# Kernel optimization log

Measured on AMD Instinct MI355X. Metric: run time of the kernel, lower is better.

The kernel has to match this reference:

```python
import jax, jax.numpy as jnp
import numpy as np
from jax import lax

FEAT_STRIDE = 16
RATIOS = np.array([0.5, 1.0, 2.0], np.float32)
SCALES = np.array([8.0, 16.0, 32.0], np.float32)
A = RATIOS.size * SCALES.size            # 9 anchors per location
N_PRE = 3000                             # pre-NMS top-k (TEST-style config)
N_POST = 300                             # post-NMS rois per image
NMS_THRESH = 0.7
MIN_SIZE = 16.0
B, C, HF, WF = 4, 512, 50, 50


def setup_inputs() -> dict:
    key = jax.random.key(0)
    ks = jax.random.split(key, 4)
    mid = 512
    return {
        "inputs": jax.random.normal(ks[0], (B, C, HF, WF), jnp.float32),
        "conv_w": jax.random.normal(ks[1], (mid, C, 3, 3), jnp.float32) * 0.01,
        "conv_b": jnp.zeros((mid,), jnp.float32),
        "bf_w": jax.random.normal(ks[2], (A * 2, mid, 1, 1), jnp.float32) * 0.01,
        "bf_b": jnp.zeros((A * 2,), jnp.float32),
        "loc_w": jax.random.normal(ks[3], (A * 4, mid, 1, 1), jnp.float32) * 0.01,
        "loc_b": jnp.zeros((A * 4,), jnp.float32),
        "img_h": 800,
        "img_w": 800,
    }


def _conv(x, w, b, pad):
    y = lax.conv_general_dilated(x, w, (1, 1), [(pad, pad), (pad, pad)],
                                 dimension_numbers=("NCHW", "OIHW", "NCHW"))
    return y + b[None, :, None, None]


def _anchors(hf, wf):
    ratios = jnp.asarray(RATIOS)
    scales = jnp.asarray(SCALES)
    hs = (FEAT_STRIDE * scales[None, :] * jnp.sqrt(ratios[:, None])).reshape(-1)
    ws = (FEAT_STRIDE * scales[None, :] * jnp.sqrt(1.0 / ratios[:, None])).reshape(-1)
    c = FEAT_STRIDE / 2.0
    base = jnp.stack([c - hs / 2, c - ws / 2, c + hs / 2, c + ws / 2], 1)  # [A,4] yxyx
    sy = jnp.arange(hf, dtype=jnp.float32) * FEAT_STRIDE
    sx = jnp.arange(wf, dtype=jnp.float32) * FEAT_STRIDE
    yy, xx = jnp.meshgrid(sy, sx, indexing="ij")
    shifts = jnp.stack([yy, xx, yy, xx], -1).reshape(-1, 1, 4)
    return (shifts + base[None]).reshape(-1, 4)  # [hf*wf*A, 4]


def _decode(anchors, loc):
    # anchors [N,4] yxyx, loc [B,N,4] (dy,dx,dh,dw)
    ah = anchors[:, 2] - anchors[:, 0]
    aw = anchors[:, 3] - anchors[:, 1]
    acy = anchors[:, 0] + 0.5 * ah
    acx = anchors[:, 1] + 0.5 * aw
    cy = loc[..., 0] * ah + acy
    cx = loc[..., 1] * aw + acx
    h = jnp.exp(loc[..., 2]) * ah
    w = jnp.exp(loc[..., 3]) * aw
    return jnp.stack([cy - 0.5 * h, cx - 0.5 * w, cy + 0.5 * h, cx + 0.5 * w], -1)


def _nms(boxes, scores):
    # boxes [N,4], scores [N] -> fixed-size [N_POST,4] rois (zero-padded)
    hs = boxes[:, 2] - boxes[:, 0]
    ws = boxes[:, 3] - boxes[:, 1]
    valid = (hs >= MIN_SIZE) & (ws >= MIN_SIZE)
    s = jnp.where(valid, scores, -jnp.inf)
    order = jnp.argsort(-s)[:N_PRE]
    b = boxes[order]
    v = valid[order]
    sb = lax.stop_gradient(b)
    area = (sb[:, 2] - sb[:, 0]) * (sb[:, 3] - sb[:, 1])
    tl = jnp.maximum(sb[:, None, :2], sb[None, :, :2])
    br = jnp.minimum(sb[:, None, 2:], sb[None, :, 2:])
    wh = jnp.clip(br - tl, 0.0)
    inter = wh[..., 0] * wh[..., 1]
    iou = inter / (area[:, None] + area[None, :] - inter + 1e-9)

    def body(i, keep):
        sup = jnp.any((iou[i] > NMS_THRESH) & keep)
        return keep.at[i].set(v[i] & ~sup)

    keep = lax.fori_loop(0, N_PRE, body, jnp.zeros((N_PRE,), bool))
    pos = jnp.where(keep, jnp.cumsum(keep) - 1, N_POST)  # invalid -> dropped
    return jnp.zeros((N_POST, 4), boxes.dtype).at[pos].set(b, mode="drop")


def reference(inputs, conv_w, conv_b, bf_w, bf_b, loc_w, loc_b, img_h, img_w):
    b_, _, hf, wf = inputs.shape
    feat = jax.nn.relu(_conv(inputs, conv_w, conv_b, 1))
    loc = _conv(feat, loc_w, loc_b, 0).transpose(0, 2, 3, 1).reshape(b_, -1, 4)
    logits = _conv(feat, bf_w, bf_b, 0).transpose(0, 2, 3, 1).reshape(b_, hf, wf, A, 2)
    probs = jax.nn.softmax(logits, axis=4)
    fg = probs[..., 1].reshape(b_, -1)             # foreground scores [B, hf*wf*A]
    bf_pred = probs.reshape(b_, -1, 2)
    anchors = _anchors(hf, wf)
    boxes = _decode(anchors, loc)
    boxes = jnp.stack([
        jnp.clip(boxes[..., 0], 0.0, img_h), jnp.clip(boxes[..., 1], 0.0, img_w),
        jnp.clip(boxes[..., 2], 0.0, img_h), jnp.clip(boxes[..., 3], 0.0, img_w)], -1)
    rois = jax.vmap(_nms)(boxes, fg).reshape(-1, 4)         # [B*N_POST, 4]
    rois_idx = jnp.repeat(jnp.arange(b_, dtype=jnp.int32), N_POST)
    return rois, rois_idx, anchors, loc, bf_pred
```

## Files before the change

### kernel.cpp

```cpp
#include <hip/hip_runtime.h>
#include <hip/hip_bf16.h>
#include <math.h>

#define BIMG   4
#define CIN    512
#define MID    512
#define HF     50
#define WF     50
#define PIX    2500
#define MTOT   10000
#define ANC    9
#define NLOC   22500
#define NPRE   3000
#define NPOST  300
#define WORDS  47
#define ROWPAD 3008
#define WSTRIDE 48
#define CAP    8192

#define ROIS_OFF 0
#define IDX_OFF  4800
#define ANC_OFF  6000
#define LOC_OFF  96000
#define BF_OFF   456000

#define WS_WT     0UL
#define WS_W1T    9437184UL
#define WS_FEAT   9568256UL
#define WS_SCORE  30048256UL
#define WS_BOXD   30768256UL
#define WS_SBD    33648256UL
#define WS_M      34032256UL
#define WS_CAND   38652544UL
#define WS_CNT    38783616UL
#define WS_PART1  38786048UL
#define WS_PART2  59266048UL
#define WS_PART3  79746048UL
#define WS_NEED2  59266048UL
#define WS_NEED4  100226048UL
#define RAWP_SZ   2560000UL

__global__ __launch_bounds__(256) void prep_kernel(
    const float* __restrict__ conv_w, const float* __restrict__ loc_w,
    const float* __restrict__ bf_w, float* __restrict__ Wt, float* __restrict__ W1t) {
  int o = blockIdx.x * 256 + threadIdx.x;
  if (o < 4608 * 512) {
    int co  = o & 511;
    int k   = o >> 9;
    int c   = k & 511;
    int tap = k >> 9;
    Wt[o] = conv_w[(co * 512 + c) * 9 + tap];
  } else {
    int o2 = o - 4608 * 512;
    if (o2 < 512 * 64) {
      int co = o2 & 63;
      int c  = o2 >> 6;
      float v = 0.0f;
      if (co < 36)      v = loc_w[co * 512 + c];
      else if (co < 54) v = bf_w[(co - 36) * 512 + c];
      W1t[o2] = v;
    }
  }
}

__device__ __forceinline__ void stage_load(
    int kb, int sg, bool in0, bool in1,
    int y0, int x0, int y1, int x1,
    const float* __restrict__ ib0, const float* __restrict__ ib1, float av[8]) {
  int tap = kb >> 5;
  int c0  = (kb & 31) << 4;
  int t3  = tap / 3;
  int dy  = t3 - 1;
  int dx  = tap - t3 * 3 - 1;
  int iy0 = y0 + dy, ix0 = x0 + dx;
  int iy1 = y1 + dy, ix1 = x1 + dx;
  bool ok0 = in0 && ((unsigned)iy0 < (unsigned)HF) && ((unsigned)ix0 < (unsigned)WF);
  bool ok1 = in1 && ((unsigned)iy1 < (unsigned)HF) && ((unsigned)ix1 < (unsigned)WF);
  int base = (c0 + sg * 4) * PIX;
  int o0 = iy0 * WF + ix0;
  int o1 = iy1 * WF + ix1;
#pragma unroll
  for (int j = 0; j < 4; ++j) {
    av[2 * j]     = ok0 ? ib0[base + j * PIX + o0] : 0.0f;
    av[2 * j + 1] = ok1 ? ib1[base + j * PIX + o1] : 0.0f;
  }
}

__global__ __launch_bounds__(256, 3) void conv3x3_kernel(
    const float* __restrict__ in, const float* __restrict__ Wt,
    float* __restrict__ part0, float* __restrict__ part1,
    float* __restrict__ part2, float* __restrict__ part3) {
  __shared__ float As[2][16][128];
  const int tid = threadIdx.x;
  const int q0 = blockIdx.x * 128;
  const int lane = tid & 63;
  const int wv = tid >> 6;
  const int col0 = __builtin_amdgcn_readfirstlane(blockIdx.y * 64 + wv * 16);
  const int half = 288 / gridDim.z;
  const int kb0 = blockIdx.z * half;
  float* __restrict__ dst = (blockIdx.z == 0) ? part0 :
                            (blockIdx.z == 1) ? part1 :
                            (blockIdx.z == 2) ? part2 : part3;

  const int sg = tid >> 6;
  const int sp = tid & 63;
  int qs0 = q0 + 2 * sp, qs1 = qs0 + 1;
  bool in0 = qs0 < MTOT, in1 = qs1 < MTOT;
  int t0 = in0 ? qs0 : 0, t1 = in1 ? qs1 : 0;
  int b0i = t0 / PIX, r0 = t0 - b0i * PIX, y0 = r0 / WF, x0 = r0 - y0 * WF;
  int b1i = t1 / PIX, r1 = t1 - b1i * PIX, y1 = r1 / WF, x1 = r1 - y1 * WF;
  const float* ib0 = in + (size_t)b0i * (CIN * PIX);
  const float* ib1 = in + (size_t)b1i * (CIN * PIX);

  double acc[2][16];
  float accf[2][16];
#pragma unroll
  for (int p = 0; p < 2; ++p)
#pragma unroll
    for (int c = 0; c < 16; ++c) { acc[p][c] = 0.0; accf[p][c] = 0.0f; }

  {
    float av[8];
    stage_load(kb0, sg, in0, in1, y0, x0, y1, x1, ib0, ib1, av);
#pragma unroll
    for (int j = 0; j < 4; ++j)
      *(float2*)&As[0][sg * 4 + j][2 * sp] = make_float2(av[2 * j], av[2 * j + 1]);
  }
  __syncthreads();

  for (int kbl = 0; kbl < half; ++kbl) {
    int kb = kb0 + kbl;
    int cur = kbl & 1;
    float av[8];
    bool has_next = (kbl + 1 < half);
    if (has_next)
      stage_load(kb + 1, sg, in0, in1, y0, x0, y1, x1, ib0, ib1, av);

    const float* __restrict__ Bw = Wt + (size_t)(kb * 16) * 512 + col0;
#pragma unroll
    for (int kg = 0; kg < 4; ++kg) {
#pragma unroll
      for (int kq = 0; kq < 4; ++kq) {
        int kk = kg * 4 + kq;
        const float* __restrict__ br = Bw + (size_t)kk * 512;
        float2 a = *(const float2*)&As[cur][kk][2 * lane];
#pragma unroll
        for (int c = 0; c < 16; ++c) {
          float bv = br[c];
          accf[0][c] = fmaf(a.x, bv, accf[0][c]);
          accf[1][c] = fmaf(a.y, bv, accf[1][c]);
        }
      }
    }
    if (kbl & 1) {
#pragma unroll
      for (int p = 0; p < 2; ++p)
#pragma unroll
        for (int c = 0; c < 16; ++c) {
          acc[p][c] += (double)accf[p][c];
          accf[p][c] = 0.0f;
        }
    }
    if (has_next) {
      int nxt = cur ^ 1;
#pragma unroll
      for (int j = 0; j < 4; ++j)
        *(float2*)&As[nxt][sg * 4 + j][2 * sp] = make_float2(av[2 * j], av[2 * j + 1]);
    }
    __syncthreads();
  }

#pragma unroll
  for (int p = 0; p < 2; ++p) {
    int q = q0 + 2 * lane + p;
    if (q < MTOT) {
      float o[16];
#pragma unroll
      for (int c = 0; c < 16; ++c) o[c] = (float)acc[p][c];
      float* fp = &dst[(size_t)q * 512 + col0];
#pragma unroll
      for (int g = 0; g < 4; ++g)
        *(float4*)&fp[g * 4] = make_float4(o[g*4], o[g*4+1], o[g*4+2], o[g*4+3]);
    }
  }
}

__global__ __launch_bounds__(256) void conv1x1_kernel(
    const float* __restrict__ p0, const float* __restrict__ p1,
    const float* __restrict__ p2, const float* __restrict__ p3, int nz,
    const float* __restrict__ convb, const float* __restrict__ W1t,
    float* __restrict__ rawp0, float* __restrict__ rawp1,
    float* __restrict__ rawp2, float* __restrict__ rawp3) {
  __shared__ float As[16][64];
  const int tid = threadIdx.x;
  const int q0 = blockIdx.x * 64;
  const int by = blockIdx.y;
  const int lane = tid & 63;
  const int wv = tid >> 6;
  const int col0 = __builtin_amdgcn_readfirstlane(wv * 16);
  float* __restrict__ rp = (by == 0) ? rawp0 : (by == 1) ? rawp1 :
                           (by == 2) ? rawp2 : rawp3;

  const int sg = tid >> 6;
  const int sp = tid & 63;
  const int qs = q0 + sp;
  const bool okL = qs < MTOT;

  double acc[16];
  float accf[16];
#pragma unroll
  for (int c = 0; c < 16; ++c) { acc[c] = 0.0; accf[c] = 0.0f; }

  for (int kbl = 0; kbl < 8; ++kbl) {
    int kb = by * 8 + kbl;
    int c0 = kb * 16;
    float fv[4] = {0.0f, 0.0f, 0.0f, 0.0f};
    if (okL) {
      const size_t base = (size_t)qs * 512 + c0 + sg * 4;
      double s[4];
      float4 a0 = *(const float4*)&p0[base];
      s[0] = (double)a0.x; s[1] = (double)a0.y; s[2] = (double)a0.z; s[3] = (double)a0.w;
      if (nz > 1) {
        float4 b0 = *(const float4*)&p1[base];
        s[0] += (double)b0.x; s[1] += (double)b0.y; s[2] += (double)b0.z; s[3] += (double)b0.w;
      }
      if (nz > 2) {
        float4 c0v = *(const float4*)&p2[base];
        s[0] += (double)c0v.x; s[1] += (double)c0v.y; s[2] += (double)c0v.z; s[3] += (double)c0v.w;
        float4 d0 = *(const float4*)&p3[base];
        s[0] += (double)d0.x; s[1] += (double)d0.y; s[2] += (double)d0.z; s[3] += (double)d0.w;
      }
      float4 bsv = *(const float4*)&convb[c0 + sg * 4];
      fv[0] = (float)fmax(s[0] + (double)bsv.x, 0.0);
      fv[1] = (float)fmax(s[1] + (double)bsv.y, 0.0);
      fv[2] = (float)fmax(s[2] + (double)bsv.z, 0.0);
      fv[3] = (float)fmax(s[3] + (double)bsv.w, 0.0);
    }
    __syncthreads();
#pragma unroll
    for (int j = 0; j < 4; ++j) As[sg * 4 + j][sp] = fv[j];
    __syncthreads();

    const float* __restrict__ Bw = W1t + (size_t)c0 * 64 + col0;
#pragma unroll
    for (int kk = 0; kk < 16; ++kk) {
      const float* __restrict__ br = Bw + (size_t)kk * 64;
      float a = As[kk][lane];
#pragma unroll
      for (int c = 0; c < 16; ++c)
        accf[c] = fmaf(a, br[c], accf[c]);
    }
    if (kbl & 1) {
#pragma unroll
      for (int c = 0; c < 16; ++c) {
        acc[c] += (double)accf[c];
        accf[c] = 0.0f;
      }
    }
  }

  int q = q0 + lane;
  if (q < MTOT) {
    float o[16];
#pragma unroll
    for (int c = 0; c < 16; ++c) o[c] = (float)acc[c];
    float* fp = &rp[(size_t)q * 64 + col0];
#pragma unroll
    for (int g = 0; g < 4; ++g)
      *(float4*)&fp[g * 4] = make_float4(o[g*4], o[g*4+1], o[g*4+2], o[g*4+3]);
  }
}

__global__ __launch_bounds__(256) void epilogue_kernel(
    const float* __restrict__ r0, const float* __restrict__ r1,
    const float* __restrict__ r2, const float* __restrict__ r3,
    const float* __restrict__ locb, const float* __restrict__ bfb,
    float* __restrict__ d_out, double* __restrict__ boxd,
    unsigned long long* __restrict__ ukey,
    const int* __restrict__ imh, const int* __restrict__ imw) {
  int idx = blockIdx.x * 256 + threadIdx.x;
  if (idx >= BIMG * NLOC) return;
  int b = idx / NLOC;
  int i = idx - b * NLOC;
  int p = i / ANC;
  int a = i - p * ANC;
  int y = p / WF;
  int x = p - y * WF;
  int q = b * PIX + p;
  const size_t rb = (size_t)q * 64;

  float4 A0 = *(const float4*)&r0[rb + a * 4];
  float4 A1 = *(const float4*)&r1[rb + a * 4];
  float4 A2 = *(const float4*)&r2[rb + a * 4];
  float4 A3 = *(const float4*)&r3[rb + a * 4];
  double l0d = (((double)A0.x + (double)A1.x) + (double)A2.x) + (double)A3.x + (double)locb[a * 4 + 0];
  double l1d = (((double)A0.y + (double)A1.y) + (double)A2.y) + (double)A3.y + (double)locb[a * 4 + 1];
  double l2d = (((double)A0.z + (double)A1.z) + (double)A2.z) + (double)A3.z + (double)locb[a * 4 + 2];
  double l3d = (((double)A0.w + (double)A1.w) + (double)A2.w) + (double)A3.w + (double)locb[a * 4 + 3];
  *(float4*)&d_out[LOC_OFF + (size_t)idx * 4] =
      make_float4((float)l0d, (float)l1d, (float)l2d, (float)l3d);

  float2 G0 = *(const float2*)&r0[rb + 36 + a * 2];
  float2 G1 = *(const float2*)&r1[rb + 36 + a * 2];
  float2 G2 = *(const float2*)&r2[rb + 36 + a * 2];
  float2 G3 = *(const float2*)&r3[rb + 36 + a * 2];
  double g0 = (((double)G0.x + (double)G1.x) + (double)G2.x) + (double)G3.x + (double)bfb[a * 2 + 0];
  double g1 = (((double)G0.y + (double)G1.y) + (double)G2.y) + (double)G3.y + (double)bfb[a * 2 + 1];
  double m  = fmax(g0, g1);
  double e0 = exp(g0 - m), e1 = exp(g1 - m);
  double s  = e0 + e1;
  double p0 = e0 / s, p1 = e1 / s;
  *(float2*)&d_out[BF_OFF + (size_t)idx * 2] = make_float2((float)p0, (float)p1);

  int ridx = a / 3, sidx = a - ridx * 3;
  double ratio = (ridx == 0) ? 0.5 : ((ridx == 1) ? 1.0 : 2.0);
  double scale = (sidx == 0) ? 8.0 : ((sidx == 1) ? 16.0 : 32.0);
  double hs = 16.0 * scale * sqrt(ratio);
  double ws = 16.0 * scale * sqrt(1.0 / ratio);
  double sy = (double)(y * 16), sx = (double)(x * 16);
  double a0 = sy + (8.0 - hs * 0.5);
  double a1 = sx + (8.0 - ws * 0.5);
  double a2 = sy + (8.0 + hs * 0.5);
  double a3 = sx + (8.0 + ws * 0.5);
  if (b == 0) {
    *(float4*)&d_out[ANC_OFF + (size_t)i * 4] =
        make_float4((float)a0, (float)a1, (float)a2, (float)a3);
  }

  double ah = a2 - a0, aw = a3 - a1;
  double acy = a0 + 0.5 * ah, acx = a1 + 0.5 * aw;
  double cy = l0d * ah + acy;
  double cx = l1d * aw + acx;
  double hh = exp(l2d) * ah;
  double ww = exp(l3d) * aw;
  double ihf = (double)imh[0], iwf = (double)imw[0];
  double b0 = fmin(fmax(cy - 0.5 * hh, 0.0), ihf);
  double b1 = fmin(fmax(cx - 0.5 * ww, 0.0), iwf);
  double b2 = fmin(fmax(cy + 0.5 * hh, 0.0), ihf);
  double b3 = fmin(fmax(cx + 0.5 * ww, 0.0), iwf);
  double* bp = &boxd[(size_t)idx * 4];
  bp[0] = b0; bp[1] = b1; bp[2] = b2; bp[3] = b3;

  bool valid = (b2 - b0 >= 16.0) && (b3 - b1 >= 16.0);
  double d = valid ? (g1 - g0) : -INFINITY;
  long long bits = __double_as_longlong(d);
  unsigned long long u = (bits < 0)
      ? ~(unsigned long long)bits
      : ((unsigned long long)bits | 0x8000000000000000ull);
  ukey[idx] = ~u;
}

__global__ __launch_bounds__(1024) void thresh_kernel(
    const unsigned long long* __restrict__ ukey,
    unsigned* __restrict__ ccnt, unsigned* __restrict__ cand) {
  __shared__ unsigned hist[16384];
  __shared__ unsigned csum[1024];
  __shared__ unsigned sT, scnt;
  int b = blockIdx.x;
  int tid = threadIdx.x;
  for (int i = tid; i < 16384; i += 1024) hist[i] = 0;
  if (tid == 0) scnt = 0;
  __syncthreads();
  for (int j = tid; j < NLOC; j += 1024)
    atomicAdd(&hist[(unsigned)(ukey[(size_t)b * NLOC + j] >> 50)], 1u);
  __syncthreads();
  unsigned s = 0;
#pragma unroll
  for (int k = 0; k < 16; ++k) s += hist[tid * 16 + k];
  csum[tid] = s;
  __syncthreads();
  if (tid == 0) {
    unsigned cum = 0;
    int T = 16383;
    for (int c = 0; c < 1024; ++c) {
      if (cum + csum[c] >= NPRE) {
        unsigned cc = cum;
        for (int k = 0; k < 16; ++k) {
          cc += hist[c * 16 + k];
          if (cc >= NPRE) { T = c * 16 + k; break; }
        }
        break;
      }
      cum += csum[c];
    }
    sT = (unsigned)T;
  }
  __syncthreads();
  unsigned T = sT;
  for (int j = tid; j < NLOC; j += 1024) {
    if ((unsigned)(ukey[(size_t)b * NLOC + j] >> 50) <= T) {
      unsigned slot = atomicAdd(&scnt, 1u);
      if (slot < CAP) cand[(size_t)b * CAP + slot] = (unsigned)j;
    }
  }
  __syncthreads();
  if (tid == 0) ccnt[b] = scnt;
}

__global__ __launch_bounds__(256) void rank_kernel(
    const unsigned long long* __restrict__ ukey, const unsigned* __restrict__ ccnt,
    const unsigned* __restrict__ cand, const double* __restrict__ boxd,
    double* __restrict__ sbd) {
  __shared__ unsigned long long kt[256];
  __shared__ unsigned it[256];
  int b = blockIdx.y;
  int C = (int)min(ccnt[b], (unsigned)CAP);
  int s = blockIdx.x * 256 + threadIdx.x;
  bool act = s < C;
  unsigned myi = act ? cand[(size_t)b * CAP + s] : 0xFFFFFFFFu;
  unsigned long long ki = act ? ukey[(size_t)b * NLOC + myi] : ~0ull;
  int cnt = 0;
  int ntile = (C + 255) >> 8;
  for (int t = 0; t < ntile; ++t) {
    int j = t * 256 + threadIdx.x;
    unsigned ji = (j < C) ? cand[(size_t)b * CAP + j] : 0xFFFFFFFFu;
    kt[threadIdx.x] = (j < C) ? ukey[(size_t)b * NLOC + ji] : ~0ull;
    it[threadIdx.x] = ji;
    __syncthreads();
#pragma unroll 8
    for (int jj = 0; jj < 256; ++jj) {
      unsigned long long kj = kt[jj];
      unsigned jidx = it[jj];
      cnt += ((kj < ki) || (kj == ki && jidx < myi)) ? 1 : 0;
    }
    __syncthreads();
  }
  if (act && cnt < NPRE) {
    const double* bx = &boxd[((size_t)b * NLOC + myi) * 4];
    double* dp = &sbd[((size_t)b * NPRE + cnt) * 4];
    dp[0] = bx[0]; dp[1] = bx[1]; dp[2] = bx[2]; dp[3] = bx[3];
  }
}

__global__ __launch_bounds__(64) void nmsmask_kernel(
    const double* __restrict__ sbd, unsigned long long* __restrict__ M) {
  __shared__ double cb[64][4];
  int b = blockIdx.z;
  int jw = blockIdx.y;
  int i  = blockIdx.x * 64 + threadIdx.x;
  int j  = jw * 64 + threadIdx.x;
  double j0 = 0, j1 = 0, j2 = 0, j3 = 0;
  if (j < NPRE) {
    const double* bp = &sbd[((size_t)b * NPRE + j) * 4];
    j0 = bp[0]; j1 = bp[1]; j2 = bp[2]; j3 = bp[3];
  }
  cb[threadIdx.x][0] = j0; cb[threadIdx.x][1] = j1;
  cb[threadIdx.x][2] = j2; cb[threadIdx.x][3] = j3;
  __syncthreads();
  if (i >= NPRE) return;
  const double* bp = &sbd[((size_t)b * NPRE + i) * 4];
  double i0 = bp[0], i1 = bp[1], i2 = bp[2], i3 = bp[3];
  double ai = (i2 - i0) * (i3 - i1);
  unsigned long long mask = 0ull;
#pragma unroll 4
  for (int t = 0; t < 64; ++t) {
    double aj = (cb[t][2] - cb[t][0]) * (cb[t][3] - cb[t][1]);
    double h = fmax(fmin(i2, cb[t][2]) - fmax(i0, cb[t][0]), 0.0);
    double w = fmax(fmin(i3, cb[t][3]) - fmax(i1, cb[t][1]), 0.0);
    double inter = h * w;
    double iou = inter / (ai + aj - inter + 1e-9);
    mask |= ((iou > 0.7) ? 1ull : 0ull) << t;
  }
  M[((size_t)b * ROWPAD + i) * WSTRIDE + jw] = mask;
}

__global__ __launch_bounds__(64) void nms_scan_kernel(
    const double* __restrict__ sbd, const unsigned long long* __restrict__ M,
    float* __restrict__ d_out) {
  int b = blockIdx.x;
  int lane = threadIdx.x;
  for (int k = lane; k < NPOST; k += 64) {
    *(float4*)&d_out[ROIS_OFF + (size_t)(b * NPOST + k) * 4] = make_float4(0, 0, 0, 0);
    d_out[IDX_OFF + b * NPOST + k] = (float)b;
  }
  __syncthreads();

  unsigned long long R = ~0ull;
  if (lane < WORDS) R = 0ull;
  for (int w = 0; w < WORDS; ++w) {
    int j = w * 64 + lane;
    bool inval = true;
    if (j < NPRE) {
      const double* bp = &sbd[((size_t)b * NPRE + j) * 4];
      double h = bp[2] - bp[0], wd = bp[3] - bp[1];
      inval = !(h >= 16.0 && wd >= 16.0);
    }
    unsigned long long bal = __ballot(inval ? 1 : 0);
    if (lane == w) R |= bal;
  }

  int kept = 0;
  while (kept < NPOST) {
    unsigned long long hz = __ballot(((~R) != 0ull) ? 1 : 0);
    if (hz == 0ull) break;
    int w0 = __ffsll(hz) - 1;
    unsigned long long word = __shfl(R, w0);
    int bit = __ffsll(~word) - 1;
    int i = w0 * 64 + bit;
    if (lane < 4)
      d_out[ROIS_OFF + (size_t)(b * NPOST + kept) * 4 + lane] =
          (float)sbd[((size_t)b * NPRE + i) * 4 + lane];
    kept++;
    if (kept >= NPOST) break;
    unsigned long long row = (lane < WORDS)
        ? M[((size_t)b * ROWPAD + i) * WSTRIDE + lane] : 0ull;
    R |= row;
    if (lane == w0) R |= (1ull << bit);
  }
}

extern "C" void kernel_launch(void* const* d_in, const int* in_sizes, int n_in,
                              void* d_out, int out_size, void* d_ws, size_t ws_size,
                              hipStream_t stream) {
  const float* in     = (const float*)d_in[0];
  const float* conv_w = (const float*)d_in[1];
  const float* conv_b = (const float*)d_in[2];
  const float* bf_w   = (const float*)d_in[3];
  const float* bf_b   = (const float*)d_in[4];
  const float* loc_w  = (const float*)d_in[5];
  const float* loc_b  = (const float*)d_in[6];
  const int*   imh    = (const int*)d_in[7];
  const int*   imw    = (const int*)d_in[8];
  float* out = (float*)d_out;

  char* ws = (char*)d_ws;
  float*  Wt    = (float*)(ws + WS_WT);
  float*  W1t   = (float*)(ws + WS_W1T);
  float*  part0 = (float*)(ws + WS_FEAT);
  unsigned long long* ukey = (unsigned long long*)(ws + WS_SCORE);
  double* boxd  = (double*)(ws + WS_BOXD);
  double* sbd   = (double*)(ws + WS_SBD);
  unsigned long long* M = (unsigned long long*)(ws + WS_M);
  unsigned* cand = (unsigned*)(ws + WS_CAND);
  unsigned* ccnt = (unsigned*)(ws + WS_CNT);
  float*  part1 = (float*)(ws + WS_PART1);
  float*  part2 = (float*)(ws + WS_PART2);
  float*  part3 = (float*)(ws + WS_PART3);
  float*  rawp0 = (float*)(ws + WS_WT);
  float*  rawp1 = (float*)(ws + WS_WT + RAWP_SZ);
  float*  rawp2 = (float*)(ws + WS_WT + 2 * RAWP_SZ);
  float*  rawp3 = (float*)(ws + WS_M);

  const int nz = (ws_size >= WS_NEED4) ? 4 : ((ws_size >= WS_NEED2) ? 2 : 1);

  hipLaunchKernelGGL(prep_kernel, dim3((4608 * 512 + 512 * 64 + 255) / 256), dim3(256),
                     0, stream, conv_w, loc_w, bf_w, Wt, W1t);
  hipLaunchKernelGGL(conv3x3_kernel, dim3(79, 8, nz), dim3(256), 0, stream,
                     in, Wt, part0, part1, part2, part3);
  hipLaunchKernelGGL(conv1x1_kernel, dim3(157, 4), dim3(256), 0, stream,
                     part0, part1, part2, part3, nz, conv_b, W1t,
                     rawp0, rawp1, rawp2, rawp3);
  hipLaunchKernelGGL(epilogue_kernel, dim3((BIMG * NLOC + 255) / 256), dim3(256), 0, stream,
                     rawp0, rawp1, rawp2, rawp3, loc_b, bf_b, out, boxd, ukey, imh, imw);
  hipLaunchKernelGGL(thresh_kernel, dim3(4), dim3(1024), 0, stream, ukey, ccnt, cand);
  hipLaunchKernelGGL(rank_kernel, dim3(CAP / 256, 4), dim3(256), 0, stream,
                     ukey, ccnt, cand, boxd, sbd);
  hipLaunchKernelGGL(nmsmask_kernel, dim3(47, 47, 4), dim3(64), 0, stream, sbd, M);
  hipLaunchKernelGGL(nms_scan_kernel, dim3(4), dim3(64), 0, stream, sbd, M, out);
}
```

Measured before the change: 1.325 ms.

## Split threshold selection into parallel hist/thresh/compact kernels and fix conv1x1 staging layout

The single 4-block thresh kernel is replaced by three kernels. A grid-wide global-atomic histogram is zeroed inside the epilogue, a small kernel picks the threshold bin, and a many-block compaction uses global atomic counters. This spreads the histogram and compaction work, which previously ran on only four workgroups, across the GPU. Separately, the conv1x1 kernel now has each group of four threads load one pixel's 16 channels for coalesced reads, and the shared tile is padded to 65 columns to avoid bank conflicts. The cost is two extra launches and contended global atomics, and the candidate order now varies between runs.

Result: slower. 1.366 ms (+3.1%).

```diff
diff --git a/kernel.cpp b/kernel.cpp
--- a/kernel.cpp
+++ b/kernel.cpp
@@ -33,12 +33,14 @@
 #define WS_M      34032256UL
 #define WS_CAND   38652544UL
 #define WS_CNT    38783616UL
+#define WS_THR    38783632UL
 #define WS_PART1  38786048UL
 #define WS_PART2  59266048UL
 #define WS_PART3  79746048UL
 #define WS_NEED2  59266048UL
 #define WS_NEED4  100226048UL
 #define RAWP_SZ   2560000UL
+#define WS_HIST   (WS_WT + 3 * RAWP_SZ)
 
 __global__ __launch_bounds__(256) void prep_kernel(
     const float* __restrict__ conv_w, const float* __restrict__ loc_w,
@@ -191,7 +193,7 @@
     const float* __restrict__ convb, const float* __restrict__ W1t,
     float* __restrict__ rawp0, float* __restrict__ rawp1,
     float* __restrict__ rawp2, float* __restrict__ rawp3) {
-  __shared__ float As[16][64];
+  __shared__ float As[16][65];
   const int tid = threadIdx.x;
   const int q0 = blockIdx.x * 64;
   const int by = blockIdx.y;
@@ -201,9 +203,9 @@
   float* __restrict__ rp = (by == 0) ? rawp0 : (by == 1) ? rawp1 :
                            (by == 2) ? rawp2 : rawp3;
 
-  const int sg = tid >> 6;
-  const int sp = tid & 63;
-  const int qs = q0 + sp;
+  const int pix = tid >> 2;
+  const int ch4 = tid & 3;
+  const int qs = q0 + pix;
   const bool okL = qs < MTOT;
 
   double acc[16];
@@ -216,7 +218,7 @@
     int c0 = kb * 16;
     float fv[4] = {0.0f, 0.0f, 0.0f, 0.0f};
     if (okL) {
-      const size_t base = (size_t)qs * 512 + c0 + sg * 4;
+      const size_t base = (size_t)qs * 512 + c0 + ch4 * 4;
       double s[4];
       float4 a0 = *(const float4*)&p0[base];
       s[0] = (double)a0.x; s[1] = (double)a0.y; s[2] = (double)a0.z; s[3] = (double)a0.w;
@@ -230,7 +232,7 @@
         float4 d0 = *(const float4*)&p3[base];
         s[0] += (double)d0.x; s[1] += (double)d0.y; s[2] += (double)d0.z; s[3] += (double)d0.w;
       }
-      float4 bsv = *(const float4*)&convb[c0 + sg * 4];
+      float4 bsv = *(const float4*)&convb[c0 + ch4 * 4];
       fv[0] = (float)fmax(s[0] + (double)bsv.x, 0.0);
       fv[1] = (float)fmax(s[1] + (double)bsv.y, 0.0);
       fv[2] = (float)fmax(s[2] + (double)bsv.z, 0.0);
@@ -238,7 +240,7 @@
     }
     __syncthreads();
 #pragma unroll
-    for (int j = 0; j < 4; ++j) As[sg * 4 + j][sp] = fv[j];
+    for (int j = 0; j < 4; ++j) As[ch4 * 4 + j][pix] = fv[j];
     __syncthreads();
 
     const float* __restrict__ Bw = W1t + (size_t)c0 * 64 + col0;
@@ -276,9 +278,10 @@
     const float* __restrict__ r2, const float* __restrict__ r3,
     const float* __restrict__ locb, const float* __restrict__ bfb,
     float* __restrict__ d_out, double* __restrict__ boxd,
-    unsigned long long* __restrict__ ukey,
+    unsigned long long* __restrict__ ukey, unsigned* __restrict__ hist,
     const int* __restrict__ imh, const int* __restrict__ imw) {
   int idx = blockIdx.x * 256 + threadIdx.x;
+  if (idx < 4 * 16384) hist[idx] = 0;
   if (idx >= BIMG * NLOC) return;
   int b = idx / NLOC;
   int i = idx - b * NLOC;
@@ -350,23 +353,24 @@
   ukey[idx] = ~u;
 }
 
-__global__ __launch_bounds__(1024) void thresh_kernel(
-    const unsigned long long* __restrict__ ukey,
-    unsigned* __restrict__ ccnt, unsigned* __restrict__ cand) {
-  __shared__ unsigned hist[16384];
+__global__ __launch_bounds__(1024) void hist_kernel(
+    const unsigned long long* __restrict__ ukey, unsigned* __restrict__ hist) {
+  int b = blockIdx.y;
+  int j = blockIdx.x * 1024 + threadIdx.x;
+  if (j < NLOC)
+    atomicAdd(&hist[b * 16384 + (unsigned)(ukey[(size_t)b * NLOC + j] >> 50)], 1u);
+}
+
+__global__ __launch_bounds__(1024) void thresh2_kernel(
+    const unsigned* __restrict__ hist,
+    unsigned* __restrict__ thr, unsigned* __restrict__ ccnt) {
   __shared__ unsigned csum[1024];
-  __shared__ unsigned sT, scnt;
   int b = blockIdx.x;
   int tid = threadIdx.x;
-  for (int i = tid; i < 16384; i += 1024) hist[i] = 0;
-  if (tid == 0) scnt = 0;
-  __syncthreads();
-  for (int j = tid; j < NLOC; j += 1024)
-    atomicAdd(&hist[(unsigned)(ukey[(size_t)b * NLOC + j] >> 50)], 1u);
-  __syncthreads();
+  const unsigned* hb = hist + b * 16384;
   unsigned s = 0;
 #pragma unroll
-  for (int k = 0; k < 16; ++k) s += hist[tid * 16 + k];
+  for (int k = 0; k < 16; ++k) s += hb[tid * 16 + k];
   csum[tid] = s;
   __syncthreads();
   if (tid == 0) {
@@ -376,25 +380,29 @@
       if (cum + csum[c] >= NPRE) {
         unsigned cc = cum;
         for (int k = 0; k < 16; ++k) {
-          cc += hist[c * 16 + k];
+          cc += hb[c * 16 + k];
           if (cc >= NPRE) { T = c * 16 + k; break; }
         }
         break;
       }
       cum += csum[c];
     }
-    sT = (unsigned)T;
-  }
-  __syncthreads();
-  unsigned T = sT;
-  for (int j = tid; j < NLOC; j += 1024) {
-    if ((unsigned)(ukey[(size_t)b * NLOC + j] >> 50) <= T) {
-      unsigned slot = atomicAdd(&scnt, 1u);
-      if (slot < CAP) cand[(size_t)b * CAP + slot] = (unsigned)j;
-    }
-  }
-  __syncthreads();
-  if (tid == 0) ccnt[b] = scnt;
+    thr[b] = (unsigned)T;
+    ccnt[b] = 0;
+  }
+}
+
+__global__ __launch_bounds__(256) void compact_kernel(
+    const unsigned long long* __restrict__ ukey, const unsigned* __restrict__ thr,
+    unsigned* __restrict__ ccnt, unsigned* __restrict__ cand) {
+  int b = blockIdx.y;
+  int i = blockIdx.x * 256 + threadIdx.x;
+  if (i >= NLOC) return;
+  unsigned T = thr[b];
+  if ((unsigned)(ukey[(size_t)b * NLOC + i] >> 50) <= T) {
+    unsigned slot = atomicAdd(&ccnt[b], 1u);
+    if (slot < CAP) cand[(size_t)b * CAP + slot] = (unsigned)i;
+  }
 }
 
 __global__ __launch_bounds__(256) void rank_kernel(
@@ -533,6 +541,7 @@
   unsigned long long* M = (unsigned long long*)(ws + WS_M);
   unsigned* cand = (unsigned*)(ws + WS_CAND);
   unsigned* ccnt = (unsigned*)(ws + WS_CNT);
+  unsigned* thr  = (unsigned*)(ws + WS_THR);
   float*  part1 = (float*)(ws + WS_PART1);
   float*  part2 = (float*)(ws + WS_PART2);
   float*  part3 = (float*)(ws + WS_PART3);
@@ -540,6 +549,7 @@
   float*  rawp1 = (float*)(ws + WS_WT + RAWP_SZ);
   float*  rawp2 = (float*)(ws + WS_WT + 2 * RAWP_SZ);
   float*  rawp3 = (float*)(ws + WS_M);
+  unsigned* hist = (unsigned*)(ws + WS_HIST);
 
   const int nz = (ws_size >= WS_NEED4) ? 4 : ((ws_size >= WS_NEED2) ? 2 : 1);
 
@@ -551,8 +561,13 @@
                      part0, part1, part2, part3, nz, conv_b, W1t,
                      rawp0, rawp1, rawp2, rawp3);
   hipLaunchKernelGGL(epilogue_kernel, dim3((BIMG * NLOC + 255) / 256), dim3(256), 0, stream,
-                     rawp0, rawp1, rawp2, rawp3, loc_b, bf_b, out, boxd, ukey, imh, imw);
-  hipLaunchKernelGGL(thresh_kernel, dim3(4), dim3(1024), 0, stream, ukey, ccnt, cand);
+                     rawp0, rawp1, rawp2, rawp3, loc_b, bf_b, out, boxd, ukey, hist,
+                     imh, imw);
+  hipLaunchKernelGGL(hist_kernel, dim3((NLOC + 1023) / 1024, 4), dim3(1024), 0, stream,
+                     ukey, hist);
+  hipLaunchKernelGGL(thresh2_kernel, dim3(4), dim3(1024), 0, stream, hist, thr, ccnt);
+  hipLaunchKernelGGL(compact_kernel, dim3(88, 4), dim3(256), 0, stream,
+                     ukey, thr, ccnt, cand);
   hipLaunchKernelGGL(rank_kernel, dim3(CAP / 256, 4), dim3(256), 0, stream,
                      ukey, ccnt, cand, boxd, sbd);
   hipLaunchKernelGGL(nmsmask_kernel, dim3(47, 47, 4), dim3(64), 0, stream, sbd, M);
```
